# Optimization experiments

Measured on AMD Instinct MI355X. Metric: run time of the kernel, lower is better.

The kernel has to match this reference:

```python
import jax, jax.numpy as jnp
import numpy as np

H = 128          # num_hidden
B = 512          # number of graphs (segments)
N0, N1, N2 = 500_000, 500_000, 250_000  # nodes per rank
EPS = 1e-5       # LayerNorm eps (torch default)


def setup_inputs() -> dict:
    key = jax.random.key(0)
    ks = jax.random.split(key, 24)
    s = 0.02
    inp = {
        "h0": jax.random.normal(ks[0], (N0, H), jnp.float32),
        "h1": jax.random.normal(ks[1], (N1, H), jnp.float32),
        "h2": jax.random.normal(ks[2], (N2, H), jnp.float32),
        "b0": jnp.sort(jax.random.randint(ks[3], (N0,), 0, B, jnp.int32)),
        "b1": jnp.sort(jax.random.randint(ks[4], (N1,), 0, B, jnp.int32)),
        "b2": jnp.sort(jax.random.randint(ks[5], (N2,), 0, B, jnp.int32)),
        "Wg0": jax.random.normal(ks[6], (H, 1), jnp.float32) * s,
        "bg0": jnp.zeros((1,), jnp.float32),
        "Wg1": jax.random.normal(ks[7], (H, 1), jnp.float32) * s,
        "bg1": jnp.zeros((1,), jnp.float32),
        "Wg2": jax.random.normal(ks[8], (H, 1), jnp.float32) * s,
        "bg2": jnp.zeros((1,), jnp.float32),
        "Wp0": jax.random.normal(ks[9], (4 * H, H), jnp.float32) * s,
        "bp0": jnp.zeros((H,), jnp.float32),
        "Wp1": jax.random.normal(ks[10], (4 * H, H), jnp.float32) * s,
        "bp1": jnp.zeros((H,), jnp.float32),
        "Wp2": jax.random.normal(ks[11], (4 * H, H), jnp.float32) * s,
        "bp2": jnp.zeros((H,), jnp.float32),
        "gamma": jnp.ones((3 * H,), jnp.float32),
        "beta": jnp.zeros((3 * H,), jnp.float32),
        "W1": jax.random.normal(ks[12], (3 * H, H), jnp.float32) * s,
        "b1f": jnp.zeros((H,), jnp.float32),
        "W2": jax.random.normal(ks[13], (H, 1), jnp.float32) * s,
        "b2f": jnp.zeros((1,), jnp.float32),
    }
    return inp


def _rank_vec(h, b, Wg, bg, Wp, bp):
    # gated multi-aggregation pooling over segments b -> [B, 4H] -> Linear -> [B, H]
    g = jax.nn.sigmoid(h @ Wg + bg)                      # [N, 1]
    sum_p = jax.ops.segment_sum(h, b, num_segments=B)    # [B, H]
    cnt = jax.ops.segment_sum(jnp.ones((h.shape[0], 1), h.dtype), b, num_segments=B)
    mean_p = sum_p / jnp.maximum(cnt, 1.0)
    max_p = jax.ops.segment_max(h, b, num_segments=B)
    max_p = jnp.where(cnt > 0, max_p, 0.0)               # guard empty segments
    gsum_p = jax.ops.segment_sum(g * h, b, num_segments=B)
    agg = jnp.concatenate([sum_p, mean_p, max_p, gsum_p], axis=1)  # [B, 4H]
    return agg @ Wp + bp


def reference(h0, h1, h2, b0, b1, b2,
              Wg0, bg0, Wg1, bg1, Wg2, bg2,
              Wp0, bp0, Wp1, bp1, Wp2, bp2,
              gamma, beta, W1, b1f, W2, b2f):
    r0 = _rank_vec(h0, b0, Wg0, bg0, Wp0, bp0)
    r1 = _rank_vec(h1, b1, Wg1, bg1, Wp1, bp1)
    r2 = _rank_vec(h2, b2, Wg2, bg2, Wp2, bp2)
    state = jnp.concatenate([r0, r1, r2], axis=1)        # [B, 3H]
    mu = jnp.mean(state, axis=-1, keepdims=True)
    var = jnp.mean(jnp.square(state - mu), axis=-1, keepdims=True)
    xn = (state - mu) * jax.lax.rsqrt(var + EPS) * gamma + beta
    x = jax.nn.silu(xn)
    x = jax.nn.silu(x @ W1 + b1f)
    out = x @ W2 + b2f                                   # [B, 1]
    return out[:, 0] if out.shape[-1] == 1 else out
```

## Files before the change

kernel.cpp:

```cpp
#include <hip/hip_runtime.h>
#include <hip/hip_bf16.h>
#include <math.h>

constexpr int H  = 128;
constexpr int B  = 512;
constexpr int RANK_STRIDE = 3 * B * H + B;
constexpr int TOTAL_WS    = 3 * RANK_STRIDE;

constexpr int ROWS_PER_WAVE  = 128;
constexpr int ROWS_PER_BLOCK = 4 * ROWS_PER_WAVE;

__device__ __forceinline__ float atomicMaxF(float* addr, float val) {
  if (val >= 0.f) {
    return __int_as_float(atomicMax((int*)addr, __float_as_int(val)));
  } else {
    return __uint_as_float(atomicMin((unsigned int*)addr, __float_as_uint(val)));
  }
}

__global__ __launch_bounds__(256) void init_ws_kernel(float* ws) {
  int i = blockIdx.x * blockDim.x + threadIdx.x;
  if (i >= TOTAL_WS) return;
  int o = i % RANK_STRIDE;
  bool ismax = (o >= 2 * B * H) && (o < 3 * B * H);
  ws[i] = ismax ? __int_as_float(0xFF800000) : 0.0f;
}

__global__ __launch_bounds__(256) void rank_fused_kernel(
    const float* __restrict__ h0, const int* __restrict__ b0,
    const float* __restrict__ Wg0, const float* __restrict__ bg0, int N0, int nb0,
    const float* __restrict__ h1, const int* __restrict__ b1,
    const float* __restrict__ Wg1, const float* __restrict__ bg1, int N1, int nb1,
    const float* __restrict__ h2, const int* __restrict__ b2,
    const float* __restrict__ Wg2, const float* __restrict__ bg2, int N2,
    float* __restrict__ ws)
{
  const int blk = blockIdx.x;
  const float* h; const int* b; const float* Wg; const float* bg;
  float* base; int N; int lblk;
  if (blk < nb0) {
    h = h0; b = b0; Wg = Wg0; bg = bg0; base = ws;                   N = N0; lblk = blk;
  } else if (blk < nb0 + nb1) {
    h = h1; b = b1; Wg = Wg1; bg = bg1; base = ws + RANK_STRIDE;     N = N1; lblk = blk - nb0;
  } else {
    h = h2; b = b2; Wg = Wg2; bg = bg2; base = ws + 2 * RANK_STRIDE; N = N2; lblk = blk - nb0 - nb1;
  }

  const int lane = threadIdx.x & 63;
  const int wv   = threadIdx.x >> 6;
  const int half = lane >> 5;
  const int c    = lane & 31;

  const int wstart = (lblk * 4 + wv) * ROWS_PER_WAVE;
  if (wstart >= N) return;
  const int wend = min(wstart + ROWS_PER_WAVE, N);

  float* __restrict__ sumb  = base;
  float* __restrict__ gsumb = base + B * H;
  float* __restrict__ maxb  = base + 2 * B * H;
  float* __restrict__ cntb  = base + 3 * B * H;

  const float4 wg  = ((const float4*)Wg)[c];
  const float  bgv = bg[0];

  const int bv0 = b[min(wstart + lane, N - 1)];
  const int bv1 = b[min(wstart + 64 + lane, N - 1)];

  float4 s  = {0.f, 0.f, 0.f, 0.f};
  float4 gq = {0.f, 0.f, 0.f, 0.f};
  float4 m  = {-INFINITY, -INFINITY, -INFINITY, -INFINITY};
  int cnt = 0;
  int cur = -1;

  auto flushLane = [&]() {
    if (cur >= 0) {
      const int bi = cur * H + c * 4;
      atomicAdd(sumb + bi + 0, s.x);  atomicAdd(sumb + bi + 1, s.y);
      atomicAdd(sumb + bi + 2, s.z);  atomicAdd(sumb + bi + 3, s.w);
      atomicAdd(gsumb + bi + 0, gq.x); atomicAdd(gsumb + bi + 1, gq.y);
      atomicAdd(gsumb + bi + 2, gq.z); atomicAdd(gsumb + bi + 3, gq.w);
      atomicMaxF(maxb + bi + 0, m.x); atomicMaxF(maxb + bi + 1, m.y);
      atomicMaxF(maxb + bi + 2, m.z); atomicMaxF(maxb + bi + 3, m.w);
      if (c == 0 && cnt) atomicAdd(cntb + cur, (float)cnt);
      s = {0.f, 0.f, 0.f, 0.f};
      gq = {0.f, 0.f, 0.f, 0.f};
      m = {-INFINITY, -INFINITY, -INFINITY, -INFINITY};
      cnt = 0;
    }
  };

  auto gateOf = [&](float4 v) -> float {
    float p = fmaf(v.x, wg.x, fmaf(v.y, wg.y, fmaf(v.z, wg.z, v.w * wg.w)));
    p += __shfl_xor(p, 1);
    p += __shfl_xor(p, 2);
    p += __shfl_xor(p, 4);
    p += __shfl_xor(p, 8);
    p += __shfl_xor(p, 16);
    return 1.0f / (1.0f + __expf(-(p + bgv)));
  };

  auto accum = [&](float4 v, float gt) {
    s.x += v.x; s.y += v.y; s.z += v.z; s.w += v.w;
    gq.x = fmaf(gt, v.x, gq.x); gq.y = fmaf(gt, v.y, gq.y);
    gq.z = fmaf(gt, v.z, gq.z); gq.w = fmaf(gt, v.w, gq.w);
    m.x = fmaxf(m.x, v.x); m.y = fmaxf(m.y, v.y);
    m.z = fmaxf(m.z, v.z); m.w = fmaxf(m.w, v.w);
  };

  const float4* __restrict__ hp = (const float4*)h;

  int r = wstart;
  while (r + 64 <= wend) {
    const int bv = (r - wstart < 64) ? bv0 : bv1;
    const int sA = __shfl(bv, 0);
    const int sB = __shfl(bv, 63);
    if (sA == sB) {
      if (sA != cur) { flushLane(); cur = sA; }
      #pragma unroll
      for (int g = 0; g < 4; ++g) {
        float4 v[8];
        #pragma unroll
        for (int i = 0; i < 8; ++i)
          v[i] = hp[(size_t)(r + g * 16 + 2 * i + half) * 32 + c];
        #pragma unroll
        for (int i = 0; i < 8; ++i) {
          const float gt = gateOf(v[i]);
          accum(v[i], gt);
        }
      }
      cnt += 32;
    } else {
      #pragma unroll 4
      for (int i = 0; i < 32; ++i) {
        const int seg = __shfl(bv, 2 * i + half);
        const float4 v = hp[(size_t)(r + 2 * i + half) * 32 + c];
        const float gt = gateOf(v);
        if (seg != cur) { flushLane(); cur = seg; }
        accum(v, gt);
        ++cnt;
      }
    }
    r += 64;
  }
  while (r + 2 <= wend) {
    const int o = r - wstart;
    const int bv = (o < 64) ? bv0 : bv1;
    const int seg = __shfl(bv, (o & 63) + half);
    const float4 v = hp[(size_t)(r + half) * 32 + c];
    const float gt = gateOf(v);
    if (seg != cur) { flushLane(); cur = seg; }
    accum(v, gt);
    ++cnt;
    r += 2;
  }
  if (r < wend) {
    const int o = r - wstart;
    const int bv = (o < 64) ? bv0 : bv1;
    const int seg = __shfl(bv, o & 63);
    const float4 v = hp[(size_t)r * 32 + c];
    const float gt = gateOf(v);
    if (half == 0) {
      if (seg != cur) { flushLane(); cur = seg; }
      accum(v, gt);
      ++cnt;
    }
  }
  flushLane();
}

__device__ __forceinline__ float siluf(float x) {
  return x / (1.0f + __expf(-x));
}

__global__ __launch_bounds__(128) void finalize_kernel(
    const float* __restrict__ ws,
    const float* __restrict__ Wp0, const float* __restrict__ bp0,
    const float* __restrict__ Wp1, const float* __restrict__ bp1,
    const float* __restrict__ Wp2, const float* __restrict__ bp2,
    const float* __restrict__ gamma, const float* __restrict__ beta,
    const float* __restrict__ W1, const float* __restrict__ b1f,
    const float* __restrict__ W2, const float* __restrict__ b2f,
    float* __restrict__ out)
{
  __shared__ float aggL[4][4 * H];
  __shared__ float state[4][3 * H];
  __shared__ float red[8];

  const int j = threadIdx.x;
  const int lane = j & 63;
  const int wv = j >> 6;
  const int gbase = blockIdx.x * 4;

  const float* Wp[3] = {Wp0, Wp1, Wp2};
  const float* bp[3] = {bp0, bp1, bp2};

  for (int k = 0; k < 3; ++k) {
    const float* sumb  = ws + k * RANK_STRIDE;
    const float* gsumb = sumb + B * H;
    const float* maxb  = sumb + 2 * B * H;
    const float* cntb  = sumb + 3 * B * H;

    for (int g = 0; g < 4; ++g) {
      const int bidx = gbase + g;
      const float cc = cntb[bidx];
      const float cm = fmaxf(cc, 1.0f);
      const float sv = sumb[bidx * H + j];
      const float mv = maxb[bidx * H + j];
      const float gv = gsumb[bidx * H + j];
      aggL[g][j]         = sv;
      aggL[g][H + j]     = sv / cm;
      aggL[g][2 * H + j] = (cc > 0.f) ? mv : 0.f;
      aggL[g][3 * H + j] = gv;
    }
    __syncthreads();

    const float bpv = bp[k][j];
    float r0 = bpv, r1 = bpv, r2 = bpv, r3 = bpv;
    const float* W = Wp[k];
    for (int i = 0; i < 4 * H; ++i) {
      const float w = W[i * H + j];
      r0 = fmaf(aggL[0][i], w, r0);
      r1 = fmaf(aggL[1][i], w, r1);
      r2 = fmaf(aggL[2][i], w, r2);
      r3 = fmaf(aggL[3][i], w, r3);
    }
    state[0][k * H + j] = r0;
    state[1][k * H + j] = r1;
    state[2][k * H + j] = r2;
    state[3][k * H + j] = r3;
    __syncthreads();
  }

  for (int g = 0; g < 4; ++g) {
    const float v0 = state[g][j];
    const float v1 = state[g][H + j];
    const float v2 = state[g][2 * H + j];
    float ps = v0 + v1 + v2;
    float pq = v0 * v0 + v1 * v1 + v2 * v2;
    for (int mm = 1; mm < 64; mm <<= 1) {
      ps += __shfl_xor(ps, mm);
      pq += __shfl_xor(pq, mm);
    }
    if (lane == 0) { red[wv * 2] = ps; red[wv * 2 + 1] = pq; }
    __syncthreads();
    const float ts = red[0] + red[2];
    const float tq = red[1] + red[3];
    const float mu  = ts * (1.0f / 384.0f);
    const float var = tq * (1.0f / 384.0f) - mu * mu;
    const float inv = rsqrtf(var + 1e-5f);
    float x0 = (v0 - mu) * inv * gamma[j]         + beta[j];
    float x1 = (v1 - mu) * inv * gamma[H + j]     + beta[H + j];
    float x2 = (v2 - mu) * inv * gamma[2 * H + j] + beta[2 * H + j];
    state[g][j]         = siluf(x0);
    state[g][H + j]     = siluf(x1);
    state[g][2 * H + j] = siluf(x2);
    __syncthreads();
  }

  const float b1v = b1f[j];
  float a0 = b1v, a1 = b1v, a2 = b1v, a3 = b1v;
  for (int i = 0; i < 3 * H; ++i) {
    const float w = W1[i * H + j];
    a0 = fmaf(state[0][i], w, a0);
    a1 = fmaf(state[1][i], w, a1);
    a2 = fmaf(state[2][i], w, a2);
    a3 = fmaf(state[3][i], w, a3);
  }
  a0 = siluf(a0); a1 = siluf(a1); a2 = siluf(a2); a3 = siluf(a3);

  const float w2 = W2[j];
  float p0 = a0 * w2, p1 = a1 * w2, p2 = a2 * w2, p3 = a3 * w2;
  for (int mm = 1; mm < 64; mm <<= 1) {
    p0 += __shfl_xor(p0, mm);
    p1 += __shfl_xor(p1, mm);
    p2 += __shfl_xor(p2, mm);
    p3 += __shfl_xor(p3, mm);
  }
  __syncthreads();
  if (lane == 0) {
    red[wv * 4 + 0] = p0; red[wv * 4 + 1] = p1;
    red[wv * 4 + 2] = p2; red[wv * 4 + 3] = p3;
  }
  __syncthreads();
  if (j < 4) out[gbase + j] = red[j] + red[4 + j] + b2f[0];
}

extern "C" void kernel_launch(void* const* d_in, const int* in_sizes, int n_in,
                              void* d_out, int out_size, void* d_ws, size_t ws_size,
                              hipStream_t stream) {
  const float* h0  = (const float*)d_in[0];
  const float* h1  = (const float*)d_in[1];
  const float* h2  = (const float*)d_in[2];
  const int*   b0  = (const int*)d_in[3];
  const int*   b1  = (const int*)d_in[4];
  const int*   b2  = (const int*)d_in[5];
  const float* Wg0 = (const float*)d_in[6];
  const float* bg0 = (const float*)d_in[7];
  const float* Wg1 = (const float*)d_in[8];
  const float* bg1 = (const float*)d_in[9];
  const float* Wg2 = (const float*)d_in[10];
  const float* bg2 = (const float*)d_in[11];
  const float* Wp0 = (const float*)d_in[12];
  const float* bp0 = (const float*)d_in[13];
  const float* Wp1 = (const float*)d_in[14];
  const float* bp1 = (const float*)d_in[15];
  const float* Wp2 = (const float*)d_in[16];
  const float* bp2 = (const float*)d_in[17];
  const float* gamma = (const float*)d_in[18];
  const float* beta  = (const float*)d_in[19];
  const float* W1  = (const float*)d_in[20];
  const float* b1f = (const float*)d_in[21];
  const float* W2  = (const float*)d_in[22];
  const float* b2f = (const float*)d_in[23];

  const int N0 = in_sizes[3];
  const int N1 = in_sizes[4];
  const int N2 = in_sizes[5];

  float* ws = (float*)d_ws;

  {
    int blocks = (TOTAL_WS + 255) / 256;
    hipLaunchKernelGGL(init_ws_kernel, dim3(blocks), dim3(256), 0, stream, ws);
  }

  const int nb0 = (N0 + ROWS_PER_BLOCK - 1) / ROWS_PER_BLOCK;
  const int nb1 = (N1 + ROWS_PER_BLOCK - 1) / ROWS_PER_BLOCK;
  const int nb2 = (N2 + ROWS_PER_BLOCK - 1) / ROWS_PER_BLOCK;
  hipLaunchKernelGGL(rank_fused_kernel, dim3(nb0 + nb1 + nb2), dim3(256), 0, stream,
                     h0, b0, Wg0, bg0, N0, nb0,
                     h1, b1, Wg1, bg1, N1, nb1,
                     h2, b2, Wg2, bg2, N2,
                     ws);

  hipLaunchKernelGGL(finalize_kernel, dim3(B / 4), dim3(128), 0, stream,
                     ws, Wp0, bp0, Wp1, bp1, Wp2, bp2,
                     gamma, beta, W1, b1f, W2, b2f, (float*)d_out);
}
```

Baseline: 793.4 us.

## Double-buffer row loads, use DPP reductions, merge half-wave partials before flush

In the uniform-segment fast path, the next 16-row group of h is now loaded into a second register buffer while the current group is being reduced, and that prefetch carries across 64-row chunks. The gate dot-product reduction replaces the __shfl_xor butterflies with DPP row operations plus a ds_swizzle. Before the final flush, the two half-waves combine their partial sum, gated sum, max and count when they hold the same segment, so only one half issues the atomics. This is meant to hide global load latency, shorten the reduction, and halve the final atomic traffic, at the cost of more registers and possibly lower occupancy.

```diff
diff --git a/kernel.cpp b/kernel.cpp
--- a/kernel.cpp
+++ b/kernel.cpp
@@ -1,5 +1,4 @@
 #include <hip/hip_runtime.h>
-#include <hip/hip_bf16.h>
 #include <math.h>
 
 constexpr int H  = 128;
@@ -24,6 +23,12 @@
   int o = i % RANK_STRIDE;
   bool ismax = (o >= 2 * B * H) && (o < 3 * B * H);
   ws[i] = ismax ? __int_as_float(0xFF800000) : 0.0f;
+}
+
+template <int CTRL>
+__device__ __forceinline__ float dpp_add(float x) {
+  int mi = __builtin_amdgcn_update_dpp(0, __float_as_int(x), CTRL, 0xF, 0xF, true);
+  return x + __int_as_float(mi);
 }
 
 __global__ __launch_bounds__(256) void rank_fused_kernel(
@@ -91,11 +96,11 @@
 
   auto gateOf = [&](float4 v) -> float {
     float p = fmaf(v.x, wg.x, fmaf(v.y, wg.y, fmaf(v.z, wg.z, v.w * wg.w)));
-    p += __shfl_xor(p, 1);
-    p += __shfl_xor(p, 2);
-    p += __shfl_xor(p, 4);
-    p += __shfl_xor(p, 8);
-    p += __shfl_xor(p, 16);
+    p = dpp_add<0xB1>(p);
+    p = dpp_add<0x4E>(p);
+    p = dpp_add<0x124>(p);
+    p = dpp_add<0x128>(p);
+    p += __int_as_float(__builtin_amdgcn_ds_swizzle(__float_as_int(p), 0x401F));
     return 1.0f / (1.0f + __expf(-(p + bgv)));
   };
 
@@ -109,6 +114,15 @@
 
   const float4* __restrict__ hp = (const float4*)h;
 
+  auto LOADB = [&](float4* dst, int baseRow) {
+    const float4* rp = hp + (size_t)baseRow * 32 + c;
+    #pragma unroll
+    for (int i = 0; i < 8; ++i) dst[i] = rp[(size_t)(2 * i + half) * 32];
+  };
+
+  float4 cbuf[8];
+  bool pre = false;
+
   int r = wstart;
   while (r + 64 <= wend) {
     const int bv = (r - wstart < 64) ? bv0 : bv1;
@@ -116,18 +130,25 @@
     const int sB = __shfl(bv, 63);
     if (sA == sB) {
       if (sA != cur) { flushLane(); cur = sA; }
+      if (!pre) LOADB(cbuf, r);
+      const bool pnext = (r + 128 <= wend);
+      float4 nbuf[8];
       #pragma unroll
       for (int g = 0; g < 4; ++g) {
-        float4 v[8];
-        #pragma unroll
-        for (int i = 0; i < 8; ++i)
-          v[i] = hp[(size_t)(r + g * 16 + 2 * i + half) * 32 + c];
+        if (g < 3) {
+          LOADB(nbuf, r + (g + 1) * 16);
+        } else if (pnext) {
+          LOADB(nbuf, r + 64);
+        }
         #pragma unroll
         for (int i = 0; i < 8; ++i) {
-          const float gt = gateOf(v[i]);
-          accum(v[i], gt);
+          const float gt = gateOf(cbuf[i]);
+          accum(cbuf[i], gt);
         }
+        #pragma unroll
+        for (int i = 0; i < 8; ++i) cbuf[i] = nbuf[i];
       }
+      pre = pnext;
       cnt += 32;
     } else {
       #pragma unroll 4
@@ -139,6 +160,7 @@
         accum(v, gt);
         ++cnt;
       }
+      pre = false;
     }
     r += 64;
   }
@@ -163,6 +185,28 @@
       if (seg != cur) { flushLane(); cur = seg; }
       accum(v, gt);
       ++cnt;
+    }
+  }
+
+  {
+    const int   ocur = __shfl_xor(cur, 32);
+    const float osx = __shfl_xor(s.x, 32), osy = __shfl_xor(s.y, 32);
+    const float osz = __shfl_xor(s.z, 32), osw = __shfl_xor(s.w, 32);
+    const float ogx = __shfl_xor(gq.x, 32), ogy = __shfl_xor(gq.y, 32);
+    const float ogz = __shfl_xor(gq.z, 32), ogw = __shfl_xor(gq.w, 32);
+    const float omx = __shfl_xor(m.x, 32), omy = __shfl_xor(m.y, 32);
+    const float omz = __shfl_xor(m.z, 32), omw = __shfl_xor(m.w, 32);
+    const int   ocnt = __shfl_xor(cnt, 32);
+    if (ocur == cur && cur >= 0) {
+      if (half == 0) {
+        s.x += osx; s.y += osy; s.z += osz; s.w += osw;
+        gq.x += ogx; gq.y += ogy; gq.z += ogz; gq.w += ogw;
+        m.x = fmaxf(m.x, omx); m.y = fmaxf(m.y, omy);
+        m.z = fmaxf(m.z, omz); m.w = fmaxf(m.w, omw);
+        cnt += ocnt;
+      } else {
+        cur = -1;
+      }
     }
   }
   flushLane();
```

After: 736.1 us. 7.2% less time.
